# Kernel tuning notes

Measured on AMD Instinct MI355X. Metric: run time of the kernel, lower is better.

Reference implementation:

```python
import jax, jax.numpy as jnp
import numpy as np

N_NODES = 10000
N_EDGES = 160000
N_GRAPHS = 20
IN_F, HID, OUT_F, HEADS = 50, 256, 121, 4
NEG_SLOPE = 0.2
GN_EPS = 1e-5
SM_EPS = 1e-16


def _with_self_loops(edge_index, n):
    loop = jnp.arange(n, dtype=edge_index.dtype)
    src = jnp.concatenate([edge_index[0], loop])
    dst = jnp.concatenate([edge_index[1], loop])
    return src, dst


def gat_conv(x, W, att_src, att_dst, bias, src, dst, heads, out_c):
    # PyG GATConv: linear -> per-node attention halves -> edge leaky_relu
    # -> softmax over incoming edges of each dst -> weighted scatter-sum.
    n = x.shape[0]
    h = (x @ W).reshape(n, heads, out_c)                # [N,H,C]
    a_s = (h * att_src).sum(-1)                          # [N,H]
    a_d = (h * att_dst).sum(-1)                          # [N,H]
    e = a_s[src] + a_d[dst]                              # [E,H]
    e = jnp.where(e > 0, e, NEG_SLOPE * e)
    e_max = jax.ops.segment_max(e, dst, num_segments=n)  # self-loops cover all dst
    ex = jnp.exp(e - e_max[dst])
    den = jax.ops.segment_sum(ex, dst, num_segments=n)
    alpha = ex / (den[dst] + SM_EPS)                     # [E,H]
    out = jax.ops.segment_sum(h[src] * alpha[..., None], dst, num_segments=n)
    return out.reshape(n, heads * out_c) + bias


def graph_norm(x, batch, weight, bias, mean_scale, n_graphs):
    cnt = jax.ops.segment_sum(jnp.ones((x.shape[0],), x.dtype), batch,
                              num_segments=n_graphs)[:, None]    # [G,1]
    mean = jax.ops.segment_sum(x, batch, num_segments=n_graphs) / cnt
    ctr = x - mean[batch] * mean_scale
    var = jax.ops.segment_sum(ctr * ctr, batch, num_segments=n_graphs) / cnt
    inv = jax.lax.rsqrt(var + GN_EPS)
    return weight * ctr * inv[batch] + bias


def setup_inputs() -> dict:
    key = jax.random.key(0)
    ks = jax.random.split(key, 24)
    d = {}
    d['x'] = jax.random.normal(ks[0], (N_NODES, IN_F), jnp.float32)
    d['edge_index'] = jax.random.randint(ks[1], (2, N_EDGES), 0, N_NODES, jnp.int64 if jax.config.jax_enable_x64 else jnp.int32)
    d['batch'] = jnp.sort(jax.random.randint(ks[2], (N_NODES,), 0, N_GRAPHS))
    def glorot(k, shape):
        fan = shape[0] + shape[-1]
        return jax.random.normal(k, shape, jnp.float32) * np.sqrt(2.0 / fan)
    dims = [(IN_F, HEADS, HID), (HEADS * HID, HEADS, HID), (HEADS * HID, HEADS, HID), (HEADS * HID, 1, OUT_F)]
    i = 3
    for li, (fin, h, c) in enumerate(dims, 1):
        d[f'W{li}'] = glorot(ks[i], (fin, h * c)); i += 1
        d[f'as{li}'] = glorot(ks[i], (h, c)); i += 1
        d[f'ad{li}'] = glorot(ks[i], (h, c)); i += 1
        d[f'b{li}'] = jnp.zeros((h * c,), jnp.float32)
    for li in (1, 2, 3):
        w = HEADS * HID
        d[f'gw{li}'] = jnp.ones((w,), jnp.float32)
        d[f'gb{li}'] = jnp.zeros((w,), jnp.float32)
        d[f'ga{li}'] = jnp.ones((w,), jnp.float32)
    return d


def reference(x, edge_index, batch,
              W1, as1, ad1, b1, W2, as2, ad2, b2, W3, as3, ad3, b3, W4, as4, ad4, b4,
              gw1, gb1, ga1, gw2, gb2, ga2, gw3, gb3, ga3):
    src, dst = _with_self_loops(edge_index, N_NODES)
    h = gat_conv(x, W1, as1, ad1, b1, src, dst, HEADS, HID)
    h = jax.nn.elu(graph_norm(h, batch, gw1, gb1, ga1, N_GRAPHS))
    h = gat_conv(h, W2, as2, ad2, b2, src, dst, HEADS, HID)
    h = jax.nn.elu(graph_norm(h, batch, gw2, gb2, ga2, N_GRAPHS))
    h = gat_conv(h, W3, as3, ad3, b3, src, dst, HEADS, HID)
    h = jax.nn.elu(graph_norm(h, batch, gw3, gb3, ga3, N_GRAPHS))
    return gat_conv(h, W4, as4, ad4, b4, src, dst, 1, OUT_F)
```

## Files before the change

kernel.cpp:

```cpp
#include <hip/hip_runtime.h>
#include <math.h>

#define NN 10000
#define NE 160000
#define E2 (NE + NN)
#define NG 20
#define MPAD 10112

typedef __attribute__((ext_vector_type(8))) short short8;
typedef __attribute__((ext_vector_type(4))) short short4v;
typedef __attribute__((ext_vector_type(4))) float f32x4;

__device__ inline unsigned short f2bf(float f){
  unsigned u = __float_as_uint(f);
  unsigned r = u + 0x7FFFu + ((u >> 16) & 1u);
  return (unsigned short)(r >> 16);
}
__device__ inline float bf2f(unsigned short h){ return __uint_as_float(((unsigned)h) << 16); }

__device__ inline void gload_lds16(const void* g, void* l){
  __builtin_amdgcn_global_load_lds((const __attribute__((address_space(1))) void*)g,
                                   (__attribute__((address_space(3))) void*)l, 16, 0, 0);
}

__global__ void k_gptr(const int* __restrict__ batch, int* __restrict__ gptr){
  int g = threadIdx.x;
  if (g > NG) return;
  int lo = 0, hi = NN;
  while (lo < hi){ int mid = (lo+hi)>>1; if (batch[mid] < g) lo = mid+1; else hi = mid; }
  gptr[g] = lo;
}

__global__ void k_count(const int* __restrict__ ei, int* __restrict__ cnt){
  int e = blockIdx.x*256 + threadIdx.x;
  if (e >= E2) return;
  int d = (e < NE) ? ei[NE + e] : (e - NE);
  atomicAdd(&cnt[d], 1);
}

__global__ void k_scan(const int* __restrict__ cnt, int* __restrict__ ptr){
  __shared__ int tpre[256];
  __shared__ int tsum[256];
  int tid = threadIdx.x;
  const int per = (NN + 255)/256;
  int base = tid*per;
  int s = 0;
  for (int i=0;i<per;i++){ int idx=base+i; if (idx<NN) s += cnt[idx]; }
  tsum[tid] = s;
  __syncthreads();
  if (tid == 0){
    int run = 0;
    for (int i=0;i<256;i++){ tpre[i]=run; run += tsum[i]; }
    ptr[NN] = run;
  }
  __syncthreads();
  int run = tpre[tid];
  for (int i=0;i<per;i++){ int idx=base+i; if (idx<NN){ ptr[idx]=run; run += cnt[idx]; } }
}

__global__ void k_copy(const int* __restrict__ src, int* __restrict__ dst){
  int i = blockIdx.x*256 + threadIdx.x;
  if (i < NN) dst[i] = src[i];
}

__global__ void k_scatter(const int* __restrict__ ei, int* __restrict__ fill, int* __restrict__ csrc){
  int e = blockIdx.x*256 + threadIdx.x;
  if (e >= E2) return;
  int s, d;
  if (e < NE){ s = ei[e]; d = ei[NE + e]; } else { s = d = e - NE; }
  int pos = atomicAdd(&fill[d], 1);
  csrc[pos] = s;
}

__global__ void k_xconv(const float* __restrict__ x, unsigned short* __restrict__ xbf){
  int i = blockIdx.x*256 + threadIdx.x;
  if (i >= MPAD*64) return;
  int r = i >> 6, c = i & 63;
  float v = (r < NN && c < 50) ? x[r*50 + c] : 0.f;
  xbf[i] = f2bf(v);
}

__global__ void k_wconv(const float* __restrict__ W, unsigned short* __restrict__ Wt,
                        int K, int N, int Kpad, int Npad){
  int i = blockIdx.x*256 + threadIdx.x;
  if (i >= Npad*Kpad) return;
  int nn = i / Kpad, kk = i - nn*Kpad;
  float v = (nn < N && kk < K) ? W[(size_t)kk*N + nn] : 0.f;
  Wt[i] = f2bf(v);
}

template<int TBM, int TBN>
__global__ __launch_bounds__(256) void k_mfma_gemm(
    const unsigned short* __restrict__ A,
    const unsigned short* __restrict__ Bt,
    unsigned short* __restrict__ Cbf,
    int M, int K, int FS, int ncb)
{
  constexpr int MFR = TBM/32;
  constexpr int NFR = TBN/32;
  constexpr int ABYTES = TBM*64;
  constexpr int BBYTES = TBN*64;
  constexpr int LPS = TBM/64 + TBN/64;
  __shared__ unsigned short sA[2*TBM*32];
  __shared__ unsigned short sB[2*TBN*32];
  const int tid = threadIdx.x;
  const int wave = tid >> 6;
  const int lane = tid & 63;
  const int nwg = gridDim.x;
  const int q = nwg >> 3, rmod = nwg & 7;
  const int xcd = blockIdx.x & 7, idx = blockIdx.x >> 3;
  const int wg = (xcd < rmod) ? (xcd*(q+1) + idx) : (rmod*(q+1) + (xcd - rmod)*q + idx);
  const int rowt = wg / ncb;
  const int colt = wg - rowt*ncb;
  const int row0 = rowt * TBM;
  const int col0 = colt * TBN;
  const int wr = (wave >> 1) * (TBM/2);
  const int wc = (wave & 1) * (TBN/2);
  f32x4 acc[MFR][NFR];
  #pragma unroll
  for (int i=0;i<MFR;i++)
    #pragma unroll
    for (int j=0;j<NFR;j++){ acc[i][j][0]=0.f; acc[i][j][1]=0.f; acc[i][j][2]=0.f; acc[i][j][3]=0.f; }

  const int arow = tid >> 2;
  const int achn = (tid & 3) ^ ((arow >> 1) & 3);
  const unsigned short* aSrc = A + (size_t)(row0 + arow)*K + achn*8;
  const unsigned short* bSrc = Bt + (size_t)(col0 + arow)*K + achn*8;
  char* ldsA = (char*)sA + wave*1024;
  char* ldsB = (char*)sB + wave*1024;

  auto STAGE = [&](int k0, int buf){
    #pragma unroll
    for (int h=0; h<TBM/64; h++) gload_lds16(aSrc + (size_t)h*64*K + k0, ldsA + buf*ABYTES + h*4096);
    #pragma unroll
    for (int h=0; h<TBN/64; h++) gload_lds16(bSrc + (size_t)h*64*K + k0, ldsB + buf*BBYTES + h*4096);
  };

  const int NT = K >> 5;
  const int kch = lane >> 4;
  const int rlo = lane & 15;

  STAGE(0, 0);
  if (NT > 1) STAGE(32, 1);
  if constexpr (LPS==4)      asm volatile("s_waitcnt vmcnt(4)" ::: "memory");
  else if constexpr (LPS==3) asm volatile("s_waitcnt vmcnt(3)" ::: "memory");
  else                       asm volatile("s_waitcnt vmcnt(2)" ::: "memory");
  __builtin_amdgcn_sched_barrier(0);
  __builtin_amdgcn_s_barrier();

  int cur = 0;
  for (int t = 0; t < NT; ++t){
    const unsigned short* bA = sA + cur*(TBM*32);
    const unsigned short* bB = sB + cur*(TBN*32);
    short8 af[MFR], bfr[NFR];
    #pragma unroll
    for (int m=0;m<MFR;m++){
      int r = wr + m*16 + rlo;
      af[m] = *(const short8*)(bA + r*32 + ((kch ^ ((r>>1)&3))<<3));
    }
    #pragma unroll
    for (int n=0;n<NFR;n++){
      int r = wc + n*16 + rlo;
      bfr[n] = *(const short8*)(bB + r*32 + ((kch ^ ((r>>1)&3))<<3));
    }
    asm volatile("s_waitcnt lgkmcnt(0)" ::: "memory");
    __builtin_amdgcn_sched_barrier(0);
    __builtin_amdgcn_s_barrier();
    if (t+2 < NT) STAGE((t+2) << 5, cur);
    #pragma unroll
    for (int m=0;m<MFR;m++)
      #pragma unroll
      for (int n=0;n<NFR;n++)
        acc[m][n] = __builtin_amdgcn_mfma_f32_16x16x32_bf16(af[m], bfr[n], acc[m][n], 0, 0, 0);
    if (t+1 < NT){
      if (t+2 < NT){
        if constexpr (LPS==4)      asm volatile("s_waitcnt vmcnt(4)" ::: "memory");
        else if constexpr (LPS==3) asm volatile("s_waitcnt vmcnt(3)" ::: "memory");
        else                       asm volatile("s_waitcnt vmcnt(2)" ::: "memory");
      } else {
        asm volatile("s_waitcnt vmcnt(0)" ::: "memory");
      }
      __builtin_amdgcn_sched_barrier(0);
      __builtin_amdgcn_s_barrier();
    }
    cur ^= 1;
  }
  const int cr = (lane >> 4) * 4;
  const int cc = lane & 15;
  #pragma unroll
  for (int m=0;m<MFR;m++){
    #pragma unroll
    for (int n=0;n<NFR;n++){
      int col = col0 + wc + n*16 + cc;
      #pragma unroll
      for (int r=0;r<4;r++){
        int row = row0 + wr + m*16 + cr + r;
        if (row < M) Cbf[(size_t)row*FS + col] = f2bf(acc[m][n][r]);
      }
    }
  }
}

__global__ __launch_bounds__(256) void k_attprepw(
    const unsigned short* __restrict__ h,
    const float* __restrict__ atts, const float* __restrict__ attd,
    float* __restrict__ a_s, float* __restrict__ a_d)
{
  const int wid = threadIdx.x >> 6, lane = threadIdx.x & 63;
  const int node = blockIdx.x*4 + wid;
  const unsigned short* hp = h + (size_t)node*1024 + lane*16;
  short8 v0 = *(const short8*)hp;
  short8 v1 = *(const short8*)(hp+8);
  const float* sp = atts + lane*16;
  const float* dp = attd + lane*16;
  float ss = 0.f, sd = 0.f;
  #pragma unroll
  for (int j=0;j<8;j++){ float f = bf2f((unsigned short)v0[j]); ss += f*sp[j];   sd += f*dp[j]; }
  #pragma unroll
  for (int j=0;j<8;j++){ float f = bf2f((unsigned short)v1[j]); ss += f*sp[8+j]; sd += f*dp[8+j]; }
  #pragma unroll
  for (int o=8;o;o>>=1){ ss += __shfl_xor(ss,o); sd += __shfl_xor(sd,o); }
  if ((lane & 15) == 0){
    int hh = lane >> 4;
    a_s[node*4 + hh] = ss;
    a_d[node*4 + hh] = sd;
  }
}

__global__ void k_attprep(const unsigned short* __restrict__ h, const float* __restrict__ atts,
                          const float* __restrict__ attd,
                          float* __restrict__ a_s, float* __restrict__ a_d, int H, int C, int FS){
  int node = blockIdx.x, head = blockIdx.y;
  int lane = threadIdx.x;
  const unsigned short* hp = h + (size_t)node*FS + head*C;
  const float* sp = atts + head*C;
  const float* dp = attd + head*C;
  float ss = 0.f, sd = 0.f;
  for (int c = lane; c < C; c += 64){ float v = bf2f(hp[c]); ss += v*sp[c]; sd += v*dp[c]; }
  #pragma unroll
  for (int o = 32; o; o >>= 1){ ss += __shfl_down(ss, o); sd += __shfl_down(sd, o); }
  if (lane == 0){ a_s[node*H + head] = ss; a_d[node*H + head] = sd; }
}

__global__ void k_alpha(const float* __restrict__ a_s, const float* __restrict__ a_d,
                        const int* __restrict__ ptr, const int* __restrict__ csrc,
                        float* __restrict__ alphaT, int H, int LH){
  int node = blockIdx.x;
  int lane = threadIdx.x;
  int beg = ptr[node], deg = ptr[node+1] - beg;
  int items = deg << LH;
  int hh = lane & (H-1);
  float ad = a_d[node*H + hh];
  float mx = -INFINITY;
  for (int i = lane; i < items; i += 64){
    int e = i >> LH;
    int s = csrc[beg + e];
    float ev = a_s[s*H + hh] + ad;
    ev = ev > 0.f ? ev : 0.2f*ev;
    mx = fmaxf(mx, ev);
  }
  for (int o = H; o < 64; o <<= 1) mx = fmaxf(mx, __shfl_xor(mx, o));
  float den = 0.f;
  for (int i = lane; i < items; i += 64){
    int e = i >> LH;
    int s = csrc[beg + e];
    float ev = a_s[s*H + hh] + ad;
    ev = ev > 0.f ? ev : 0.2f*ev;
    den += __expf(ev - mx);
  }
  for (int o = H; o < 64; o <<= 1) den += __shfl_xor(den, o);
  float inv = 1.f / (den + 1e-16f);
  for (int i = lane; i < items; i += 64){
    int e = i >> LH;
    int s = csrc[beg + e];
    float ev = a_s[s*H + hh] + ad;
    ev = ev > 0.f ? ev : 0.2f*ev;
    alphaT[(size_t)hh*E2 + beg + e] = __expf(ev - mx) * inv;
  }
}

__global__ __launch_bounds__(256) void k_gatherw(
    const unsigned short* __restrict__ h,
    const float* __restrict__ a_s, const float* __restrict__ a_d,
    const int* __restrict__ ptr, const int* __restrict__ csrc,
    const float* __restrict__ bias, float* __restrict__ out)
{
  __shared__ float sal[4][64*4];
  __shared__ int ssn[4][64];
  const int wid = threadIdx.x >> 6, lane = threadIdx.x & 63;
  const int node = blockIdx.x*4 + wid;
  const int hh = lane >> 4;
  const int beg = ptr[node], deg = ptr[node+1] - beg;
  f32x4 ad4 = *(const f32x4*)(a_d + node*4);
  float acc[16], acc2[16];
  #pragma unroll
  for (int j=0;j<16;j++){ acc[j]=0.f; acc2[j]=0.f; }
  f32x4 denp = {0.f,0.f,0.f,0.f};
  const unsigned short* hb = h + lane*16;

  for (int c0 = 0; c0 < deg; c0 += 64){
    int n = min(64, deg - c0);
    if (lane < n){
      int s = csrc[beg + c0 + lane];
      f32x4 as4 = *(const f32x4*)(a_s + s*4);
      f32x4 e4;
      #pragma unroll
      for (int k2=0;k2<4;k2++){
        float ev = as4[k2] + ad4[k2];
        ev = ev > 0.f ? ev : 0.2f*ev;
        float x = __expf(ev);
        e4[k2] = x;
        denp[k2] += x;
      }
      *(f32x4*)&sal[wid][lane*4] = e4;
      ssn[wid][lane] = s;
    }
    int e = 0;
    for (; e + 1 < n; e += 2){
      int sA_ = ssn[wid][e], sB_ = ssn[wid][e+1];
      float aA = sal[wid][e*4 + hh], aB = sal[wid][(e+1)*4 + hh];
      const unsigned short* pA = hb + (size_t)sA_*1024;
      const unsigned short* pB = hb + (size_t)sB_*1024;
      short8 uA0 = *(const short8*)pA, uA1 = *(const short8*)(pA+8);
      short8 uB0 = *(const short8*)pB, uB1 = *(const short8*)(pB+8);
      #pragma unroll
      for (int j=0;j<8;j++){ acc[j]   += bf2f((unsigned short)uA0[j])*aA;
                             acc[8+j] += bf2f((unsigned short)uA1[j])*aA; }
      #pragma unroll
      for (int j=0;j<8;j++){ acc2[j]   += bf2f((unsigned short)uB0[j])*aB;
                             acc2[8+j] += bf2f((unsigned short)uB1[j])*aB; }
    }
    if (e < n){
      int sA_ = ssn[wid][e];
      float aA = sal[wid][e*4 + hh];
      const unsigned short* pA = hb + (size_t)sA_*1024;
      short8 uA0 = *(const short8*)pA, uA1 = *(const short8*)(pA+8);
      #pragma unroll
      for (int j=0;j<8;j++){ acc[j]   += bf2f((unsigned short)uA0[j])*aA;
                             acc[8+j] += bf2f((unsigned short)uA1[j])*aA; }
    }
  }
  #pragma unroll
  for (int o=32;o;o>>=1){
    #pragma unroll
    for (int k2=0;k2<4;k2++) denp[k2] += __shfl_xor(denp[k2], o);
  }
  float inv = 1.f / (denp[hh] + 1e-16f);
  float* op = out + (size_t)node*1024 + lane*16;
  const float* bp = bias + lane*16;
  #pragma unroll
  for (int j=0;j<16;j++) op[j] = (acc[j]+acc2[j])*inv + bp[j];
}

template<int L>
__global__ __launch_bounds__(256) void k_gather2(
    const unsigned short* __restrict__ h, int FS,
    const float* __restrict__ alphaT,
    const int* __restrict__ ptr, const int* __restrict__ csrc,
    const float* __restrict__ bias, float* __restrict__ out,
    int F, int C, int outF)
{
  constexpr int NGRP = 256 / L;
  constexpr int CS = L * 8;
  const int node = blockIdx.x;
  const int head = blockIdx.y;
  const int colbase = head * C;
  const int beg = ptr[node], deg = ptr[node+1] - beg;
  __shared__ int ssrc[256];
  __shared__ float salv[256];
  __shared__ float red[NGRP * CS];
  const int tid = threadIdx.x;
  const int grp = tid / L, li = tid % L;
  const int c0 = colbase + li*8;
  const float* aT = alphaT + (size_t)head*E2 + beg;
  float acc[8] = {0.f,0.f,0.f,0.f,0.f,0.f,0.f,0.f};
  for (int b0 = 0; b0 < deg; b0 += 256){
    int bn = min(256, deg - b0);
    if (tid < bn){ ssrc[tid] = csrc[beg + b0 + tid]; salv[tid] = aT[b0 + tid]; }
    __syncthreads();
    for (int e = grp; e < bn; e += NGRP){
      int s = ssrc[e];
      float al = salv[e];
      short8 v = *(const short8*)(h + (size_t)s*FS + c0);
      #pragma unroll
      for (int j=0;j<8;j++) acc[j] += bf2f((unsigned short)v[j]) * al;
    }
    __syncthreads();
  }
  #pragma unroll
  for (int j=0;j<8;j++) red[grp*CS + li*8 + j] = acc[j];
  __syncthreads();
  for (int c = tid; c < CS; c += 256){
    float s = 0.f;
    #pragma unroll
    for (int g=0; g<NGRP; g++) s += red[g*CS + c];
    int oc = colbase + c;
    if (oc < F) out[(size_t)node*outF + oc] = s + bias[oc];
  }
}

#define NSPLIT 16
__global__ void k_gnstats(const float* __restrict__ x, const int* __restrict__ gptr,
                          float* __restrict__ gsum, float* __restrict__ gsq, int F){
  int g = blockIdx.x, cc = blockIdx.y, sp = blockIdx.z;
  int c = cc*256 + threadIdx.x;
  if (c >= F) return;
  int beg = gptr[g], end = gptr[g+1];
  int n = end - beg;
  int per = (n + NSPLIT - 1) / NSPLIT;
  int nb = beg + sp*per, ne = min(end, nb + per);
  if (ne <= nb) return;
  float s = 0.f, q = 0.f;
  for (int i = nb; i < ne; i++){ float v = x[(size_t)i*F + c]; s += v; q += v*v; }
  atomicAdd(&gsum[g*F + c], s);
  atomicAdd(&gsq[g*F + c], q);
}

__global__ void k_coef(const float* __restrict__ gsum, const float* __restrict__ gsq, const int* __restrict__ gptr,
                       const float* __restrict__ w, const float* __restrict__ b, const float* __restrict__ ms,
                       float* __restrict__ cA, float* __restrict__ cB, int F){
  int i = blockIdx.x*256 + threadIdx.x;
  if (i >= NG*F) return;
  int g = i / F, c = i - g*F;
  float cntf = (float)(gptr[g+1] - gptr[g]);
  float m = gsum[i] / cntf;
  float s = ms[c];
  float ex2 = gsq[i] / cntf;
  float var = ex2 - 2.f*s*m*m + s*s*m*m;
  float inv = rsqrtf(var + 1e-5f);
  float wa = w[c]*inv;
  cA[i] = wa;
  cB[i] = b[c] - wa*m*s;
}

__global__ void k_applyelu(const float* __restrict__ x, const int* __restrict__ batch,
                           const float* __restrict__ cA, const float* __restrict__ cB,
                           unsigned short* __restrict__ obf, int F){
  size_t i = (size_t)blockIdx.x*256 + threadIdx.x;
  if (i >= (size_t)NN*F) return;
  int node = (int)(i / F);
  int c = (int)(i - (size_t)node*F);
  int g = batch[node];
  float y = cA[g*F + c]*x[i] + cB[g*F + c];
  y = y > 0.f ? y : expm1f(y);
  obf[i] = f2bf(y);
}

extern "C" void kernel_launch(void* const* d_in, const int* in_sizes, int n_in,
                              void* d_out, int out_size, void* d_ws, size_t ws_size,
                              hipStream_t stream){
  (void)in_sizes; (void)n_in; (void)out_size; (void)ws_size;
  const float* x     = (const float*)d_in[0];
  const int*   ei    = (const int*)d_in[1];
  const int*   batch = (const int*)d_in[2];
  const float* W[4]  = {(const float*)d_in[3],  (const float*)d_in[7],  (const float*)d_in[11], (const float*)d_in[15]};
  const float* AS[4] = {(const float*)d_in[4],  (const float*)d_in[8],  (const float*)d_in[12], (const float*)d_in[16]};
  const float* AD[4] = {(const float*)d_in[5],  (const float*)d_in[9],  (const float*)d_in[13], (const float*)d_in[17]};
  const float* BI[4] = {(const float*)d_in[6],  (const float*)d_in[10], (const float*)d_in[14], (const float*)d_in[18]};
  const float* GW[3] = {(const float*)d_in[19], (const float*)d_in[22], (const float*)d_in[25]};
  const float* GB[3] = {(const float*)d_in[20], (const float*)d_in[23], (const float*)d_in[26]};
  const float* GA[3] = {(const float*)d_in[21], (const float*)d_in[24], (const float*)d_in[27]};

  float* ws   = (float*)d_ws;
  float* bufB = ws;
  float* a_s  = bufB + (size_t)NN*1024;
  float* a_d  = a_s + (size_t)NN*4;
  float* gsum = a_d + (size_t)NN*4;
  float* gsq  = gsum + (size_t)NG*1024;
  float* cA   = gsq  + (size_t)NG*1024;
  float* cB   = cA   + (size_t)NG*1024;
  float* alphaT = cB + (size_t)NG*1024;
  int* ptr  = (int*)(alphaT + (size_t)4*E2);
  int* fill = ptr + (NN + 8);
  int* csrc = fill + (NN + 8);
  int* gptr = csrc + E2;
  unsigned short* xbf = (unsigned short*)(gptr + 24);
  unsigned short* abf = xbf + (size_t)MPAD*64;
  unsigned short* hbf = abf + (size_t)MPAD*1024;
  unsigned short* Wt  = hbf + (size_t)NN*1024;

  hipMemsetAsync(fill, 0, sizeof(int)*(NN+1), stream);
  k_gptr<<<1, 32, 0, stream>>>(batch, gptr);
  k_count<<<(E2+255)/256, 256, 0, stream>>>(ei, fill);
  k_scan<<<1, 256, 0, stream>>>(fill, ptr);
  k_copy<<<(NN+255)/256, 256, 0, stream>>>(ptr, fill);
  k_scatter<<<(E2+255)/256, 256, 0, stream>>>(ei, fill, csrc);
  k_xconv<<<(MPAD*64+255)/256, 256, 0, stream>>>(x, xbf);

  const int Kp[4]  = {64, 1024, 1024, 1024};
  const int Kr[4]  = {50, 1024, 1024, 1024};
  const int Np[4]  = {1024, 1024, 1024, 128};
  for (int li = 0; li < 4; ++li){
    int H = (li == 3) ? 1 : 4;
    int LH = (li == 3) ? 0 : 2;
    int C = (li == 3) ? 121 : 256;
    int F = H*C;
    int FS = Np[li];
    const unsigned short* Ain = (li == 0) ? xbf : abf;
    k_wconv<<<(Np[li]*Kp[li]+255)/256, 256, 0, stream>>>(W[li], Wt, Kr[li], F, Kp[li], Np[li]);
    if (li < 3){
      int ncb = Np[li]/128;
      int nwg = (MPAD/64) * ncb;
      k_mfma_gemm<64,128><<<nwg, 256, 0, stream>>>(Ain, Wt, hbf, NN, Kp[li], FS, ncb);
      k_attprepw<<<NN/4, 256, 0, stream>>>(hbf, AS[li], AD[li], a_s, a_d);
      k_gatherw<<<NN/4, 256, 0, stream>>>(hbf, a_s, a_d, ptr, csrc, BI[li], bufB);
      hipMemsetAsync(gsum, 0, sizeof(float)*2*NG*1024, stream);
      k_gnstats<<<dim3(NG, (F+255)/256, NSPLIT), 256, 0, stream>>>(bufB, gptr, gsum, gsq, F);
      k_coef<<<(NG*F + 255)/256, 256, 0, stream>>>(gsum, gsq, gptr, GW[li], GB[li], GA[li], cA, cB, F);
      size_t tot = (size_t)NN*F;
      k_applyelu<<<(unsigned)((tot + 255)/256), 256, 0, stream>>>(bufB, batch, cA, cB, abf, F);
    } else {
      int ncb = Np[li]/64;
      int nwg = (MPAD/64) * ncb;
      k_mfma_gemm<64,64><<<nwg, 256, 0, stream>>>(Ain, Wt, hbf, NN, Kp[li], FS, ncb);
      k_attprep<<<dim3(NN, 1), 64, 0, stream>>>(hbf, AS[li], AD[li], a_s, a_d, H, C, FS);
      k_alpha<<<NN, 64, 0, stream>>>(a_s, a_d, ptr, csrc, alphaT, H, LH);
      k_gather2<16><<<dim3(NN, 1), 256, 0, stream>>>(hbf, FS, alphaT, ptr, csrc, BI[li], (float*)d_out, F, C, F);
    }
  }
}
```

Measured before the change: 519.0 us.

## Triple-buffer GEMM, fuse final-layer softmax into gather, batch weight conversion

The GEMM moves from double to triple LDS buffering. It uses a single barrier per k-step and raises wave priority around the MFMA block. The last layer's separate attprep, alpha and gather kernels are replaced by a per-wave attprep and a fused gather that computes the softmax weights inline, which removes the alphaT round trip. Weight conversions for all layers run in one launch, and the GraphNorm stats write per-split partials instead of using atomics plus a memset. The fused gather skips max subtraction in the softmax, so large logits could overflow exp. It is also missing a __syncthreads-free guarantee between LDS writes and reads within a wave.

```diff
diff --git a/kernel.cpp b/kernel.cpp
--- a/kernel.cpp
+++ b/kernel.cpp
@@ -6,9 +6,9 @@
 #define E2 (NE + NN)
 #define NG 20
 #define MPAD 10112
+#define NSPLIT 8
 
 typedef __attribute__((ext_vector_type(8))) short short8;
-typedef __attribute__((ext_vector_type(4))) short short4v;
 typedef __attribute__((ext_vector_type(4))) float f32x4;
 
 __device__ inline unsigned short f2bf(float f){
@@ -80,13 +80,25 @@
   xbf[i] = f2bf(v);
 }
 
-__global__ void k_wconv(const float* __restrict__ W, unsigned short* __restrict__ Wt,
-                        int K, int N, int Kpad, int Npad){
+#define WT0 0
+#define WT1 65536
+#define WT2 1114112
+#define WT3 2162688
+#define WTT 2293760
+__global__ void k_wconvall(const float* __restrict__ W0, const float* __restrict__ W1,
+                           const float* __restrict__ W2, const float* __restrict__ W3,
+                           unsigned short* __restrict__ wt){
   int i = blockIdx.x*256 + threadIdx.x;
-  if (i >= Npad*Kpad) return;
-  int nn = i / Kpad, kk = i - nn*Kpad;
+  if (i >= WTT) return;
+  const float* W; int K, N, Kpad, off;
+  if (i < WT1){ W=W0; K=50; N=1024; Kpad=64; off=WT0; }
+  else if (i < WT2){ W=W1; K=1024; N=1024; Kpad=1024; off=WT1; }
+  else if (i < WT3){ W=W2; K=1024; N=1024; Kpad=1024; off=WT2; }
+  else { W=W3; K=1024; N=121; Kpad=1024; off=WT3; }
+  int j = i - off;
+  int nn = j / Kpad, kk = j - nn*Kpad;
   float v = (nn < N && kk < K) ? W[(size_t)kk*N + nn] : 0.f;
-  Wt[i] = f2bf(v);
+  wt[i] = f2bf(v);
 }
 
 template<int TBM, int TBN>
@@ -101,8 +113,8 @@
   constexpr int ABYTES = TBM*64;
   constexpr int BBYTES = TBN*64;
   constexpr int LPS = TBM/64 + TBN/64;
-  __shared__ unsigned short sA[2*TBM*32];
-  __shared__ unsigned short sB[2*TBN*32];
+  __shared__ unsigned short sA[3*TBM*32];
+  __shared__ unsigned short sB[3*TBN*32];
   const int tid = threadIdx.x;
   const int wave = tid >> 6;
   const int lane = tid & 63;
@@ -141,15 +153,21 @@
   const int rlo = lane & 15;
 
   STAGE(0, 0);
-  if (NT > 1) STAGE(32, 1);
-  if constexpr (LPS==4)      asm volatile("s_waitcnt vmcnt(4)" ::: "memory");
-  else if constexpr (LPS==3) asm volatile("s_waitcnt vmcnt(3)" ::: "memory");
-  else                       asm volatile("s_waitcnt vmcnt(2)" ::: "memory");
-  __builtin_amdgcn_sched_barrier(0);
-  __builtin_amdgcn_s_barrier();
+  STAGE(32, 1);
 
   int cur = 0;
   for (int t = 0; t < NT; ++t){
+    asm volatile("s_waitcnt lgkmcnt(0)" ::: "memory");
+    if (t+1 < NT){
+      if constexpr (LPS==4)      asm volatile("s_waitcnt vmcnt(4)" ::: "memory");
+      else if constexpr (LPS==3) asm volatile("s_waitcnt vmcnt(3)" ::: "memory");
+      else                       asm volatile("s_waitcnt vmcnt(2)" ::: "memory");
+    } else {
+      asm volatile("s_waitcnt vmcnt(0)" ::: "memory");
+    }
+    __builtin_amdgcn_sched_barrier(0);
+    __builtin_amdgcn_s_barrier();
+    __builtin_amdgcn_sched_barrier(0);
     const unsigned short* bA = sA + cur*(TBM*32);
     const unsigned short* bB = sB + cur*(TBN*32);
     short8 af[MFR], bfr[NFR];
@@ -163,27 +181,18 @@
       int r = wc + n*16 + rlo;
       bfr[n] = *(const short8*)(bB + r*32 + ((kch ^ ((r>>1)&3))<<3));
     }
-    asm volatile("s_waitcnt lgkmcnt(0)" ::: "memory");
-    __builtin_amdgcn_sched_barrier(0);
-    __builtin_amdgcn_s_barrier();
-    if (t+2 < NT) STAGE((t+2) << 5, cur);
+    if (t+2 < NT){
+      int nb = cur + 2; if (nb >= 3) nb -= 3;
+      STAGE((t+2) << 5, nb);
+    }
+    __builtin_amdgcn_s_setprio(1);
     #pragma unroll
     for (int m=0;m<MFR;m++)
       #pragma unroll
       for (int n=0;n<NFR;n++)
         acc[m][n] = __builtin_amdgcn_mfma_f32_16x16x32_bf16(af[m], bfr[n], acc[m][n], 0, 0, 0);
-    if (t+1 < NT){
-      if (t+2 < NT){
-        if constexpr (LPS==4)      asm volatile("s_waitcnt vmcnt(4)" ::: "memory");
-        else if constexpr (LPS==3) asm volatile("s_waitcnt vmcnt(3)" ::: "memory");
-        else                       asm volatile("s_waitcnt vmcnt(2)" ::: "memory");
-      } else {
-        asm volatile("s_waitcnt vmcnt(0)" ::: "memory");
-      }
-      __builtin_amdgcn_sched_barrier(0);
-      __builtin_amdgcn_s_barrier();
-    }
-    cur ^= 1;
+    __builtin_amdgcn_s_setprio(0);
+    cur += 1; if (cur == 3) cur = 0;
   }
   const int cr = (lane >> 4) * 4;
   const int cc = lane & 15;
@@ -227,56 +236,27 @@
   }
 }
 
-__global__ void k_attprep(const unsigned short* __restrict__ h, const float* __restrict__ atts,
-                          const float* __restrict__ attd,
-                          float* __restrict__ a_s, float* __restrict__ a_d, int H, int C, int FS){
-  int node = blockIdx.x, head = blockIdx.y;
-  int lane = threadIdx.x;
-  const unsigned short* hp = h + (size_t)node*FS + head*C;
-  const float* sp = atts + head*C;
-  const float* dp = attd + head*C;
+__global__ __launch_bounds__(256) void k_attprep4(
+    const unsigned short* __restrict__ h,
+    const float* __restrict__ atts, const float* __restrict__ attd,
+    float* __restrict__ a_s, float* __restrict__ a_d)
+{
+  const int wid = threadIdx.x >> 6, lane = threadIdx.x & 63;
+  const int node = blockIdx.x*4 + wid;
+  const unsigned short* hp = h + (size_t)node*128;
   float ss = 0.f, sd = 0.f;
-  for (int c = lane; c < C; c += 64){ float v = bf2f(hp[c]); ss += v*sp[c]; sd += v*dp[c]; }
-  #pragma unroll
-  for (int o = 32; o; o >>= 1){ ss += __shfl_down(ss, o); sd += __shfl_down(sd, o); }
-  if (lane == 0){ a_s[node*H + head] = ss; a_d[node*H + head] = sd; }
-}
-
-__global__ void k_alpha(const float* __restrict__ a_s, const float* __restrict__ a_d,
-                        const int* __restrict__ ptr, const int* __restrict__ csrc,
-                        float* __restrict__ alphaT, int H, int LH){
-  int node = blockIdx.x;
-  int lane = threadIdx.x;
-  int beg = ptr[node], deg = ptr[node+1] - beg;
-  int items = deg << LH;
-  int hh = lane & (H-1);
-  float ad = a_d[node*H + hh];
-  float mx = -INFINITY;
-  for (int i = lane; i < items; i += 64){
-    int e = i >> LH;
-    int s = csrc[beg + e];
-    float ev = a_s[s*H + hh] + ad;
-    ev = ev > 0.f ? ev : 0.2f*ev;
-    mx = fmaxf(mx, ev);
-  }
-  for (int o = H; o < 64; o <<= 1) mx = fmaxf(mx, __shfl_xor(mx, o));
-  float den = 0.f;
-  for (int i = lane; i < items; i += 64){
-    int e = i >> LH;
-    int s = csrc[beg + e];
-    float ev = a_s[s*H + hh] + ad;
-    ev = ev > 0.f ? ev : 0.2f*ev;
-    den += __expf(ev - mx);
-  }
-  for (int o = H; o < 64; o <<= 1) den += __shfl_xor(den, o);
-  float inv = 1.f / (den + 1e-16f);
-  for (int i = lane; i < items; i += 64){
-    int e = i >> LH;
-    int s = csrc[beg + e];
-    float ev = a_s[s*H + hh] + ad;
-    ev = ev > 0.f ? ev : 0.2f*ev;
-    alphaT[(size_t)hh*E2 + beg + e] = __expf(ev - mx) * inv;
-  }
+  {
+    float f = bf2f(hp[lane]);
+    if (lane < 121){ ss += f*atts[lane]; sd += f*attd[lane]; }
+  }
+  int c2 = lane + 64;
+  if (c2 < 121){
+    float f = bf2f(hp[c2]);
+    ss += f*atts[c2]; sd += f*attd[c2];
+  }
+  #pragma unroll
+  for (int o=32;o;o>>=1){ ss += __shfl_xor(ss,o); sd += __shfl_xor(sd,o); }
+  if (lane == 0){ a_s[node] = ss; a_d[node] = sd; }
 }
 
 __global__ __launch_bounds__(256) void k_gatherw(
@@ -352,80 +332,88 @@
   for (int j=0;j<16;j++) op[j] = (acc[j]+acc2[j])*inv + bp[j];
 }
 
-template<int L>
-__global__ __launch_bounds__(256) void k_gather2(
-    const unsigned short* __restrict__ h, int FS,
-    const float* __restrict__ alphaT,
+__global__ __launch_bounds__(256) void k_gatherw1(
+    const unsigned short* __restrict__ h,
+    const float* __restrict__ a_s, const float* __restrict__ a_d,
     const int* __restrict__ ptr, const int* __restrict__ csrc,
-    const float* __restrict__ bias, float* __restrict__ out,
-    int F, int C, int outF)
+    const float* __restrict__ bias, float* __restrict__ out)
 {
-  constexpr int NGRP = 256 / L;
-  constexpr int CS = L * 8;
-  const int node = blockIdx.x;
-  const int head = blockIdx.y;
-  const int colbase = head * C;
+  __shared__ float sal[4][64];
+  __shared__ int ssn[4][64];
+  const int wid = threadIdx.x >> 6, lane = threadIdx.x & 63;
+  const int node = blockIdx.x*4 + wid;
   const int beg = ptr[node], deg = ptr[node+1] - beg;
-  __shared__ int ssrc[256];
-  __shared__ float salv[256];
-  __shared__ float red[NGRP * CS];
-  const int tid = threadIdx.x;
-  const int grp = tid / L, li = tid % L;
-  const int c0 = colbase + li*8;
-  const float* aT = alphaT + (size_t)head*E2 + beg;
-  float acc[8] = {0.f,0.f,0.f,0.f,0.f,0.f,0.f,0.f};
-  for (int b0 = 0; b0 < deg; b0 += 256){
-    int bn = min(256, deg - b0);
-    if (tid < bn){ ssrc[tid] = csrc[beg + b0 + tid]; salv[tid] = aT[b0 + tid]; }
-    __syncthreads();
-    for (int e = grp; e < bn; e += NGRP){
-      int s = ssrc[e];
-      float al = salv[e];
-      short8 v = *(const short8*)(h + (size_t)s*FS + c0);
-      #pragma unroll
-      for (int j=0;j<8;j++) acc[j] += bf2f((unsigned short)v[j]) * al;
-    }
-    __syncthreads();
-  }
-  #pragma unroll
-  for (int j=0;j<8;j++) red[grp*CS + li*8 + j] = acc[j];
-  __syncthreads();
-  for (int c = tid; c < CS; c += 256){
-    float s = 0.f;
-    #pragma unroll
-    for (int g=0; g<NGRP; g++) s += red[g*CS + c];
-    int oc = colbase + c;
-    if (oc < F) out[(size_t)node*outF + oc] = s + bias[oc];
-  }
-}
-
-#define NSPLIT 16
+  float ad = a_d[node];
+  float den = 0.f;
+  float acc[2] = {0.f,0.f}, acc2[2] = {0.f,0.f};
+  const int c0i = lane*2;
+  const unsigned short* hb = h + c0i;
+
+  for (int b0 = 0; b0 < deg; b0 += 64){
+    int n = min(64, deg - b0);
+    if (lane < n){
+      int s = csrc[beg + b0 + lane];
+      float ev = a_s[s] + ad;
+      ev = ev > 0.f ? ev : 0.2f*ev;
+      float x = __expf(ev);
+      sal[wid][lane] = x;
+      ssn[wid][lane] = s;
+      den += x;
+    }
+    int e = 0;
+    for (; e + 1 < n; e += 2){
+      int sA_ = ssn[wid][e], sB_ = ssn[wid][e+1];
+      float aA = sal[wid][e], aB = sal[wid][e+1];
+      const unsigned short* pA = hb + (size_t)sA_*128;
+      const unsigned short* pB = hb + (size_t)sB_*128;
+      acc[0]  += bf2f(pA[0])*aA; acc[1]  += bf2f(pA[1])*aA;
+      acc2[0] += bf2f(pB[0])*aB; acc2[1] += bf2f(pB[1])*aB;
+    }
+    if (e < n){
+      int sA_ = ssn[wid][e];
+      float aA = sal[wid][e];
+      const unsigned short* pA = hb + (size_t)sA_*128;
+      acc[0] += bf2f(pA[0])*aA; acc[1] += bf2f(pA[1])*aA;
+    }
+  }
+  #pragma unroll
+  for (int o=32;o;o>>=1) den += __shfl_xor(den, o);
+  float inv = 1.f / (den + 1e-16f);
+  if (c0i < 121)   out[(size_t)node*121 + c0i]   = (acc[0]+acc2[0])*inv + bias[c0i];
+  if (c0i+1 < 121) out[(size_t)node*121 + c0i+1] = (acc[1]+acc2[1])*inv + bias[c0i+1];
+}
+
 __global__ void k_gnstats(const float* __restrict__ x, const int* __restrict__ gptr,
-                          float* __restrict__ gsum, float* __restrict__ gsq, int F){
+                          float* __restrict__ psum, float* __restrict__ psq){
   int g = blockIdx.x, cc = blockIdx.y, sp = blockIdx.z;
   int c = cc*256 + threadIdx.x;
-  if (c >= F) return;
   int beg = gptr[g], end = gptr[g+1];
   int n = end - beg;
   int per = (n + NSPLIT - 1) / NSPLIT;
   int nb = beg + sp*per, ne = min(end, nb + per);
-  if (ne <= nb) return;
-  float s = 0.f, q = 0.f;
-  for (int i = nb; i < ne; i++){ float v = x[(size_t)i*F + c]; s += v; q += v*v; }
-  atomicAdd(&gsum[g*F + c], s);
-  atomicAdd(&gsq[g*F + c], q);
-}
-
-__global__ void k_coef(const float* __restrict__ gsum, const float* __restrict__ gsq, const int* __restrict__ gptr,
+  float s = 0.f, qv = 0.f;
+  for (int i = nb; i < ne; i++){ float v = x[(size_t)i*1024 + c]; s += v; qv += v*v; }
+  int idx = (sp*NG + g)*1024 + c;
+  psum[idx] = s; psq[idx] = qv;
+}
+
+__global__ void k_coef(const float* __restrict__ psum, const float* __restrict__ psq,
+                       const int* __restrict__ gptr,
                        const float* __restrict__ w, const float* __restrict__ b, const float* __restrict__ ms,
-                       float* __restrict__ cA, float* __restrict__ cB, int F){
+                       float* __restrict__ cA, float* __restrict__ cB){
   int i = blockIdx.x*256 + threadIdx.x;
-  if (i >= NG*F) return;
-  int g = i / F, c = i - g*F;
+  if (i >= NG*1024) return;
+  int g = i >> 10, c = i & 1023;
   float cntf = (float)(gptr[g+1] - gptr[g]);
-  float m = gsum[i] / cntf;
+  float sm = 0.f, sq = 0.f;
+  #pragma unroll
+  for (int sp=0; sp<NSPLIT; sp++){
+    sm += psum[(sp*NG + g)*1024 + c];
+    sq += psq[(sp*NG + g)*1024 + c];
+  }
+  float m = sm / cntf;
   float s = ms[c];
-  float ex2 = gsq[i] / cntf;
+  float ex2 = sq / cntf;
   float var = ex2 - 2.f*s*m*m + s*s*m*m;
   float inv = rsqrtf(var + 1e-5f);
   float wa = w[c]*inv;
@@ -435,13 +423,13 @@
 
 __global__ void k_applyelu(const float* __restrict__ x, const int* __restrict__ batch,
                            const float* __restrict__ cA, const float* __restrict__ cB,
-                           unsigned short* __restrict__ obf, int F){
+                           unsigned short* __restrict__ obf){
   size_t i = (size_t)blockIdx.x*256 + threadIdx.x;
-  if (i >= (size_t)NN*F) return;
-  int node = (int)(i / F);
-  int c = (int)(i - (size_t)node*F);
+  if (i >= (size_t)NN*1024) return;
+  int node = (int)(i >> 10);
+  int c = (int)(i & 1023);
   int g = batch[node];
-  float y = cA[g*F + c]*x[i] + cB[g*F + c];
+  float y = cA[g*1024 + c]*x[i] + cB[g*1024 + c];
   y = y > 0.f ? y : expm1f(y);
   obf[i] = f2bf(y);
 }
@@ -465,19 +453,18 @@
   float* bufB = ws;
   float* a_s  = bufB + (size_t)NN*1024;
   float* a_d  = a_s + (size_t)NN*4;
-  float* gsum = a_d + (size_t)NN*4;
-  float* gsq  = gsum + (size_t)NG*1024;
-  float* cA   = gsq  + (size_t)NG*1024;
+  float* psum = a_d + (size_t)NN*4;
+  float* psq  = psum + (size_t)NSPLIT*NG*1024;
+  float* cA   = psq  + (size_t)NSPLIT*NG*1024;
   float* cB   = cA   + (size_t)NG*1024;
-  float* alphaT = cB + (size_t)NG*1024;
-  int* ptr  = (int*)(alphaT + (size_t)4*E2);
+  int* ptr  = (int*)(cB + (size_t)NG*1024);
   int* fill = ptr + (NN + 8);
   int* csrc = fill + (NN + 8);
   int* gptr = csrc + E2;
-  unsigned short* xbf = (unsigned short*)(gptr + 24);
-  unsigned short* abf = xbf + (size_t)MPAD*64;
+  unsigned short* abf = (unsigned short*)(gptr + 24);
+  unsigned short* xbf = abf;
   unsigned short* hbf = abf + (size_t)MPAD*1024;
-  unsigned short* Wt  = hbf + (size_t)NN*1024;
+  unsigned short* wt  = hbf + (size_t)NN*1024;
 
   hipMemsetAsync(fill, 0, sizeof(int)*(NN+1), stream);
   k_gptr<<<1, 32, 0, stream>>>(batch, gptr);
@@ -486,36 +473,30 @@
   k_copy<<<(NN+255)/256, 256, 0, stream>>>(ptr, fill);
   k_scatter<<<(E2+255)/256, 256, 0, stream>>>(ei, fill, csrc);
   k_xconv<<<(MPAD*64+255)/256, 256, 0, stream>>>(x, xbf);
+  k_wconvall<<<(WTT+255)/256, 256, 0, stream>>>(W[0], W[1], W[2], W[3], wt);
 
   const int Kp[4]  = {64, 1024, 1024, 1024};
-  const int Kr[4]  = {50, 1024, 1024, 1024};
   const int Np[4]  = {1024, 1024, 1024, 128};
+  const int Woff[4] = {WT0, WT1, WT2, WT3};
   for (int li = 0; li < 4; ++li){
-    int H = (li == 3) ? 1 : 4;
-    int LH = (li == 3) ? 0 : 2;
-    int C = (li == 3) ? 121 : 256;
-    int F = H*C;
     int FS = Np[li];
     const unsigned short* Ain = (li == 0) ? xbf : abf;
-    k_wconv<<<(Np[li]*Kp[li]+255)/256, 256, 0, stream>>>(W[li], Wt, Kr[li], F, Kp[li], Np[li]);
+    const unsigned short* Wt = wt + Woff[li];
     if (li < 3){
       int ncb = Np[li]/128;
       int nwg = (MPAD/64) * ncb;
       k_mfma_gemm<64,128><<<nwg, 256, 0, stream>>>(Ain, Wt, hbf, NN, Kp[li], FS, ncb);
       k_attprepw<<<NN/4, 256, 0, stream>>>(hbf, AS[li], AD[li], a_s, a_d);
       k_gatherw<<<NN/4, 256, 0, stream>>>(hbf, a_s, a_d, ptr, csrc, BI[li], bufB);
-      hipMemsetAsync(gsum, 0, sizeof(float)*2*NG*1024, stream);
-      k_gnstats<<<dim3(NG, (F+255)/256, NSPLIT), 256, 0, stream>>>(bufB, gptr, gsum, gsq, F);
-      k_coef<<<(NG*F + 255)/256, 256, 0, stream>>>(gsum, gsq, gptr, GW[li], GB[li], GA[li], cA, cB, F);
-      size_t tot = (size_t)NN*F;
-      k_applyelu<<<(unsigned)((tot + 255)/256), 256, 0, stream>>>(bufB, batch, cA, cB, abf, F);
+      k_gnstats<<<dim3(NG, 4, NSPLIT), 256, 0, stream>>>(bufB, gptr, psum, psq);
+      k_coef<<<(NG*1024 + 255)/256, 256, 0, stream>>>(psum, psq, gptr, GW[li], GB[li], GA[li], cA, cB);
+      k_applyelu<<<(NN*1024 + 255)/256, 256, 0, stream>>>(bufB, batch, cA, cB, abf);
     } else {
       int ncb = Np[li]/64;
       int nwg = (MPAD/64) * ncb;
       k_mfma_gemm<64,64><<<nwg, 256, 0, stream>>>(Ain, Wt, hbf, NN, Kp[li], FS, ncb);
-      k_attprep<<<dim3(NN, 1), 64, 0, stream>>>(hbf, AS[li], AD[li], a_s, a_d, H, C, FS);
-      k_alpha<<<NN, 64, 0, stream>>>(a_s, a_d, ptr, csrc, alphaT, H, LH);
-      k_gather2<16><<<dim3(NN, 1), 256, 0, stream>>>(hbf, FS, alphaT, ptr, csrc, BI[li], (float*)d_out, F, C, F);
-    }
-  }
-}
+      k_attprep4<<<NN/4, 256, 0, stream>>>(hbf, AS[li], AD[li], a_s, a_d);
+      k_gatherw1<<<NN/4, 256, 0, stream>>>(hbf, a_s, a_d, ptr, csrc, BI[li], (float*)d_out);
+    }
+  }
+}
```

New measurement: 516.2 us. No clear change (-0.5%).
